# Optimization experiments

Hardware: AMD Instinct MI355X
Metric: run time of the kernel (lower is better)

The kernel has to match this reference:

```python
import jax, jax.numpy as jnp
import numpy as np

ALPHA1 = 1.0
ALPHA2 = 1.0
MARGIN = 0.5
NORM_EPS = 1e-12   # torch F.normalize eps
LOG_CLAMP = -100.0 # torch BCELoss clamps log to -100


def _hausdorff(X, Y):
    # X: [Lx, B, D], Y: [Ly, B, D]
    Xn = X / jnp.maximum(jnp.sqrt(jnp.sum(X * X, axis=-1, keepdims=True)), NORM_EPS)
    Yn = Y / jnp.maximum(jnp.sqrt(jnp.sum(Y * Y, axis=-1, keepdims=True)), NORM_EPS)
    dot = jnp.einsum('xbd,ybd->xyb', Xn, Yn)            # [Lx, Ly, B]
    dist = jnp.sqrt(jnp.maximum(2.0 - 2.0 * dot, 0.0))  # [Lx, Ly, B]
    d_X_Y = dist.min(axis=1).max(axis=0)  # [B]
    d_Y_X = dist.min(axis=0).max(axis=0)  # [B]
    return jnp.maximum(d_X_Y, d_Y_X)[:, None]  # [B, 1]


def setup_inputs() -> dict:
    key = jax.random.key(0)
    k1, k2, k3, k4, k5, k6 = jax.random.split(key, 6)
    Lx, Ly, B, D = 512, 128, 64, 512
    Bm, M = 64, 32
    encoded_frame = jax.random.normal(k1, (Lx, B, D), dtype=jnp.float32)
    encoded_word = jax.random.normal(k2, (Ly, B, D), dtype=jnp.float32)
    predict_mask_feature = jax.random.normal(k3, (Bm, M, D), dtype=jnp.float32)
    masked_feature = jax.random.normal(k4, (Bm, M, D), dtype=jnp.float32)
    prob_v = jnp.clip(jax.random.uniform(k5, (B, 1), dtype=jnp.float32), 1e-4, 1.0 - 1e-4)
    label = jax.random.randint(k6, (B,), 0, 2, dtype=jnp.int64)
    return {
        'encoded_frame': encoded_frame,
        'encoded_word': encoded_word,
        'predict_mask_feature': predict_mask_feature,
        'masked_feature': masked_feature,
        'prob_v': prob_v,
        'label': label,
    }


def reference(encoded_frame, encoded_word, predict_mask_feature, masked_feature, prob_v, label):
    label_v = label.astype(jnp.float32)[:, None]  # [B, 1]
    hd = _hausdorff(encoded_frame, encoded_word)  # [B, 1]
    mask_predict_loss = jnp.mean((predict_mask_feature - masked_feature) ** 2)
    contrast_loss = jnp.mean(
        label_v * hd ** 2 + (1.0 - label_v) * jax.nn.relu(MARGIN - hd) ** 2
    )
    logp = jnp.maximum(jnp.log(prob_v), LOG_CLAMP)
    log1mp = jnp.maximum(jnp.log1p(-prob_v), LOG_CLAMP)
    bce_loss = -jnp.mean(label_v * logp + (1.0 - label_v) * log1mp)
    loss = bce_loss + ALPHA1 * mask_predict_loss + ALPHA2 * contrast_loss
    return loss
```

## Files before the change

### kernel.cpp

```cpp
#include <hip/hip_runtime.h>
#include <hip/hip_bf16.h>
#include <math.h>

#define BB 64
#define DD 512
#define NMSE (64*32*512)
#define NGEMM 512
#define NMSEB 64
#define BK 64
#define PAD 72
#define KITERS (DD/BK)

typedef __attribute__((ext_vector_type(8)))  short v8s;
typedef __attribute__((ext_vector_type(16))) float v16f;

__device__ inline unsigned short bfb(float f) {
    union { __hip_bfloat16 h; unsigned short s; } u;
    u.h = __float2bfloat16(f);
    return u.s;
}
__device__ inline float bff(unsigned short s) { return __uint_as_float(((unsigned)s) << 16); }

__device__ inline void cvt_store(float4 v, unsigned short* __restrict__ H,
                                 unsigned short* __restrict__ L, int off, float& ssq) {
    ssq = fmaf(v.x, v.x, ssq); ssq = fmaf(v.y, v.y, ssq);
    ssq = fmaf(v.z, v.z, ssq); ssq = fmaf(v.w, v.w, ssq);
    unsigned short h0 = bfb(v.x), h1 = bfb(v.y), h2 = bfb(v.z), h3 = bfb(v.w);
    float l0 = v.x - bff(h0), l1 = v.y - bff(h1), l2 = v.z - bff(h2), l3 = v.w - bff(h3);
    uint2 hp, lp;
    hp.x = (unsigned)h0 | ((unsigned)h1 << 16);
    hp.y = (unsigned)h2 | ((unsigned)h3 << 16);
    lp.x = (unsigned)bfb(l0) | ((unsigned)bfb(l1) << 16);
    lp.y = (unsigned)bfb(l2) | ((unsigned)bfb(l3) << 16);
    *(uint2*)&H[off] = hp;
    *(uint2*)&L[off] = lp;
}

__device__ inline void bar_lds() {
    asm volatile("s_waitcnt lgkmcnt(0)" ::: "memory");
    __builtin_amdgcn_s_barrier();
    asm volatile("" ::: "memory");
}

__global__ __launch_bounds__(512, 4) void k_main(const float* __restrict__ X,
                                                 const float* __restrict__ Y,
                                                 const float* __restrict__ P,
                                                 const float* __restrict__ M,
                                                 float* __restrict__ pm1,
                                                 float* __restrict__ pcm,
                                                 float* __restrict__ msep) {
    __shared__ unsigned short Ah[64 * PAD], Al[64 * PAD];
    __shared__ unsigned short Bh[128 * PAD], Bl[128 * PAD];
    __shared__ float sSqX[64], sSqY[128];
    __shared__ float rowm[4][64];
    __shared__ float colm[2][128];
    __shared__ float sred[512];

    int tid = threadIdx.x;

    if (blockIdx.x >= NGEMM) {
        const float4* p4 = (const float4*)P;
        const float4* m4 = (const float4*)M;
        int n4 = NMSE / 4;
        float s = 0.0f;
        for (int i = (blockIdx.x - NGEMM) * 512 + tid; i < n4; i += NMSEB * 512) {
            float4 a = p4[i], b = m4[i];
            float dx = a.x - b.x, dy = a.y - b.y, dz = a.z - b.z, dw = a.w - b.w;
            s += dx*dx + dy*dy + dz*dz + dw*dw;
        }
        sred[tid] = s;
        __syncthreads();
        for (int o = 256; o > 0; o >>= 1) {
            if (tid < o) sred[tid] += sred[tid + o];
            __syncthreads();
        }
        if (tid == 0) msep[blockIdx.x - NGEMM] = sred[0];
        return;
    }

    int d  = blockIdx.x;
    int g  = d & 7;
    int s_ = d >> 3;
    int b  = g * 8 + (s_ & 7);
    int xt = s_ >> 3;
    int x0 = xt * 64;

    int w    = tid >> 6;
    int wr   = w >> 2;
    int wc   = w & 3;
    int lane = tid & 63;
    int ln31 = lane & 31;
    int hi   = lane >> 5;
    int g8   = hi * 8;
    int arow = 32 * wr + ln31;
    int bcol = 32 * wc + ln31;

    int r  = tid >> 4;
    int q  = tid & 15;
    const float* gA0 = &X[((size_t)(x0 + r) * BB + b) * DD + q * 4];
    const float* gA1 = &X[((size_t)(x0 + r + 32) * BB + b) * DD + q * 4];
    const float* gB0 = &Y[((size_t)(r)      * BB + b) * DD + q * 4];
    const float* gB1 = &Y[((size_t)(r + 32) * BB + b) * DD + q * 4];
    const float* gB2 = &Y[((size_t)(r + 64) * BB + b) * DD + q * 4];
    const float* gB3 = &Y[((size_t)(r + 96) * BB + b) * DD + q * 4];

    v16f acc;
    #pragma unroll
    for (int t = 0; t < 16; ++t) acc[t] = 0.0f;
    float sqA0 = 0.0f, sqA1 = 0.0f, sqB0 = 0.0f, sqB1 = 0.0f, sqB2 = 0.0f, sqB3 = 0.0f;

    float4 pa0 = *(const float4*)(gA0);
    float4 pa1 = *(const float4*)(gA1);
    float4 pb0 = *(const float4*)(gB0);
    float4 pb1 = *(const float4*)(gB1);
    float4 pb2 = *(const float4*)(gB2);
    float4 pb3 = *(const float4*)(gB3);

    for (int it = 0; it < KITERS; ++it) {
        cvt_store(pa0, Ah, Al, (r)      * PAD + q * 4, sqA0);
        cvt_store(pa1, Ah, Al, (r + 32) * PAD + q * 4, sqA1);
        cvt_store(pb0, Bh, Bl, (r)      * PAD + q * 4, sqB0);
        cvt_store(pb1, Bh, Bl, (r + 32) * PAD + q * 4, sqB1);
        cvt_store(pb2, Bh, Bl, (r + 64) * PAD + q * 4, sqB2);
        cvt_store(pb3, Bh, Bl, (r + 96) * PAD + q * 4, sqB3);
        bar_lds();

        if (it < KITERS - 1) {
            int k0 = (it + 1) * BK;
            pa0 = *(const float4*)(gA0 + k0);
            pa1 = *(const float4*)(gA1 + k0);
            pb0 = *(const float4*)(gB0 + k0);
            pb1 = *(const float4*)(gB1 + k0);
            pb2 = *(const float4*)(gB2 + k0);
            pb3 = *(const float4*)(gB3 + k0);
        }

        #pragma unroll
        for (int ks = 0; ks < 4; ++ks) {
            int koff = ks * 16 + g8;
            v8s ah = *(const v8s*)&Ah[arow * PAD + koff];
            v8s al = *(const v8s*)&Al[arow * PAD + koff];
            v8s bh = *(const v8s*)&Bh[bcol * PAD + koff];
            v8s bl = *(const v8s*)&Bl[bcol * PAD + koff];
            acc = __builtin_amdgcn_mfma_f32_32x32x16_bf16(ah, bh, acc, 0, 0, 0);
            acc = __builtin_amdgcn_mfma_f32_32x32x16_bf16(ah, bl, acc, 0, 0, 0);
            acc = __builtin_amdgcn_mfma_f32_32x32x16_bf16(al, bh, acc, 0, 0, 0);
        }
        bar_lds();
    }

    #pragma unroll
    for (int o = 1; o < 16; o <<= 1) {
        sqA0 += __shfl_xor(sqA0, o, 64);
        sqA1 += __shfl_xor(sqA1, o, 64);
        sqB0 += __shfl_xor(sqB0, o, 64);
        sqB1 += __shfl_xor(sqB1, o, 64);
        sqB2 += __shfl_xor(sqB2, o, 64);
        sqB3 += __shfl_xor(sqB3, o, 64);
    }
    if (q == 0) {
        sSqX[r]      = sqA0;  sSqX[r + 32] = sqA1;
        sSqY[r]      = sqB0;  sSqY[r + 32] = sqB1;
        sSqY[r + 64] = sqB2;  sSqY[r + 96] = sqB3;
    }
    __syncthreads();
    if (tid < 64) sSqX[tid] = 1.0f / fmaxf(sqrtf(sSqX[tid]), 1e-12f);
    else if (tid < 192) sSqY[tid - 64] = 1.0f / fmaxf(sqrtf(sSqY[tid - 64]), 1e-12f);
    __syncthreads();

    float sy = sSqY[32 * wc + ln31];
    #pragma unroll
    for (int t = 0; t < 16; ++t) {
        float sx = sSqX[32 * wr + (t & 3) + 8 * (t >> 2) + 4 * hi];
        acc[t] *= sx * sy;
    }

    #pragma unroll
    for (int t = 0; t < 16; ++t) {
        float m = acc[t];
        #pragma unroll
        for (int o = 1; o < 32; o <<= 1) m = fmaxf(m, __shfl_xor(m, o, 64));
        if (ln31 == 0) {
            int rowid = (t & 3) + 8 * (t >> 2) + 4 * hi;
            rowm[wc][32 * wr + rowid] = m;
        }
    }

    float cm = acc[0];
    #pragma unroll
    for (int t = 1; t < 16; ++t) cm = fmaxf(cm, acc[t]);
    cm = fmaxf(cm, __shfl_xor(cm, 32, 64));
    if (lane < 32) colm[wr][32 * wc + lane] = cm;
    __syncthreads();

    if (tid < 64) {
        float v = fmaxf(fmaxf(rowm[0][tid], rowm[1][tid]),
                        fmaxf(rowm[2][tid], rowm[3][tid]));
        #pragma unroll
        for (int o = 1; o < 64; o <<= 1) v = fminf(v, __shfl_xor(v, o, 64));
        if (tid == 0) pm1[b * 8 + xt] = v;
    }
    if (tid >= 64 && tid < 192) {
        int c = tid - 64;
        pcm[(size_t)(b * 8 + xt) * 128 + c] = fmaxf(colm[0][c], colm[1][c]);
    }
}

__global__ __launch_bounds__(256) void k_red(const float* __restrict__ pm1,
                                             const float* __restrict__ pcm,
                                             const float* __restrict__ prob,
                                             const int* __restrict__ label,
                                             float* __restrict__ lossb) {
    __shared__ float red[128];
    int tid = threadIdx.x;
    int b = blockIdx.x;

    if (tid < 128) {
        float cm = -1e30f;
        #pragma unroll
        for (int t = 0; t < 8; ++t)
            cm = fmaxf(cm, pcm[(size_t)(b * 8 + t) * 128 + tid]);
        red[tid] = cm;
    }
    __syncthreads();
    if (tid < 64) {
        float v = fminf(red[tid], red[tid + 64]);
        #pragma unroll
        for (int o = 1; o < 64; o <<= 1) v = fminf(v, __shfl_xor(v, o, 64));
        if (tid == 0) {
            float m1 = 1e30f;
            #pragma unroll
            for (int t = 0; t < 8; ++t) m1 = fminf(m1, pm1[b * 8 + t]);
            float m = fminf(m1, v);
            float hd = sqrtf(fmaxf(2.0f - 2.0f * m, 0.0f));
            float lab = (float)label[b];
            float rel = fmaxf(0.5f - hd, 0.0f);
            float contrast = lab * hd * hd + (1.0f - lab) * rel * rel;
            float pv = prob[b];
            float logp   = fmaxf(logf(pv), -100.0f);
            float log1mp = fmaxf(log1pf(-pv), -100.0f);
            float bce = -(lab * logp + (1.0f - lab) * log1mp);
            lossb[b] = contrast + bce;
        }
    }
}

__global__ __launch_bounds__(64) void k_fin(const float* __restrict__ lossb,
                                            const float* __restrict__ msep,
                                            float* __restrict__ out) {
    int tid = threadIdx.x;
    float v = lossb[tid] * (1.0f / 64.0f) + msep[tid] * (1.0f / (float)NMSE);
    #pragma unroll
    for (int o = 32; o > 0; o >>= 1) v += __shfl_down(v, o, 64);
    if (tid == 0) out[0] = v;
}

extern "C" void kernel_launch(void* const* d_in, const int* in_sizes, int n_in,
                              void* d_out, int out_size, void* d_ws, size_t ws_size,
                              hipStream_t stream) {
    const float* X = (const float*)d_in[0];
    const float* Y = (const float*)d_in[1];
    const float* P = (const float*)d_in[2];
    const float* M = (const float*)d_in[3];
    const float* pv = (const float*)d_in[4];
    const int*   lb = (const int*)d_in[5];
    float* out = (float*)d_out;

    float* ws = (float*)d_ws;
    float* pm1   = ws;
    float* pcm   = ws + 512;
    float* msep  = ws + 66048;
    float* lossb = ws + 66112;

    k_main<<<NGEMM + NMSEB, 512, 0, stream>>>(X, Y, P, M, pm1, pcm, msep);
    k_red<<<BB, 256, 0, stream>>>(pm1, pcm, pv, lb, lossb);
    k_fin<<<1, 64, 0, stream>>>(lossb, msep, out);
}
```

Measured before the change: 129.5 us.

## Double-buffer global prefetch in GEMM loop and fuse final reduction via atomics

The main GEMM loop now keeps two K-tiles of global loads in flight, using two register sets and a manually unrolled pair of iterations, so that load latency overlaps more of the LDS conversion and MFMA work. The final single-block reduction kernel is removed: the output is zeroed inside k_main, and each k_red2 block atomically adds its scaled contribution, saving one kernel launch. This costs more registers, which may reduce occupancy under launch_bounds(512,4), and makes the floating-point summation order nondeterministic.

```diff
diff --git a/kernel.cpp b/kernel.cpp
--- a/kernel.cpp
+++ b/kernel.cpp
@@ -48,7 +48,8 @@
                                                  const float* __restrict__ M,
                                                  float* __restrict__ pm1,
                                                  float* __restrict__ pcm,
-                                                 float* __restrict__ msep) {
+                                                 float* __restrict__ msep,
+                                                 float* __restrict__ out) {
     __shared__ unsigned short Ah[64 * PAD], Al[64 * PAD];
     __shared__ unsigned short Bh[128 * PAD], Bl[128 * PAD];
     __shared__ float sSqX[64], sSqY[128];
@@ -59,6 +60,7 @@
     int tid = threadIdx.x;
 
     if (blockIdx.x >= NGEMM) {
+        if (blockIdx.x == NGEMM && tid == 0) out[0] = 0.0f;
         const float4* p4 = (const float4*)P;
         const float4* m4 = (const float4*)M;
         int n4 = NMSE / 4;
@@ -109,32 +111,28 @@
     for (int t = 0; t < 16; ++t) acc[t] = 0.0f;
     float sqA0 = 0.0f, sqA1 = 0.0f, sqB0 = 0.0f, sqB1 = 0.0f, sqB2 = 0.0f, sqB3 = 0.0f;
 
-    float4 pa0 = *(const float4*)(gA0);
-    float4 pa1 = *(const float4*)(gA1);
-    float4 pb0 = *(const float4*)(gB0);
-    float4 pb1 = *(const float4*)(gB1);
-    float4 pb2 = *(const float4*)(gB2);
-    float4 pb3 = *(const float4*)(gB3);
-
-    for (int it = 0; it < KITERS; ++it) {
-        cvt_store(pa0, Ah, Al, (r)      * PAD + q * 4, sqA0);
-        cvt_store(pa1, Ah, Al, (r + 32) * PAD + q * 4, sqA1);
-        cvt_store(pb0, Bh, Bl, (r)      * PAD + q * 4, sqB0);
-        cvt_store(pb1, Bh, Bl, (r + 32) * PAD + q * 4, sqB1);
-        cvt_store(pb2, Bh, Bl, (r + 64) * PAD + q * 4, sqB2);
-        cvt_store(pb3, Bh, Bl, (r + 96) * PAD + q * 4, sqB3);
-        bar_lds();
-
-        if (it < KITERS - 1) {
-            int k0 = (it + 1) * BK;
-            pa0 = *(const float4*)(gA0 + k0);
-            pa1 = *(const float4*)(gA1 + k0);
-            pb0 = *(const float4*)(gB0 + k0);
-            pb1 = *(const float4*)(gB1 + k0);
-            pb2 = *(const float4*)(gB2 + k0);
-            pb3 = *(const float4*)(gB3 + k0);
-        }
-
+    float4 p0a0 = *(const float4*)(gA0), p0a1 = *(const float4*)(gA1);
+    float4 p0b0 = *(const float4*)(gB0), p0b1 = *(const float4*)(gB1);
+    float4 p0b2 = *(const float4*)(gB2), p0b3 = *(const float4*)(gB3);
+    float4 p1a0 = *(const float4*)(gA0 + BK), p1a1 = *(const float4*)(gA1 + BK);
+    float4 p1b0 = *(const float4*)(gB0 + BK), p1b1 = *(const float4*)(gB1 + BK);
+    float4 p1b2 = *(const float4*)(gB2 + BK), p1b3 = *(const float4*)(gB3 + BK);
+
+    #pragma unroll
+    for (int it = 0; it < KITERS; it += 2) {
+        cvt_store(p0a0, Ah, Al, (r)      * PAD + q * 4, sqA0);
+        cvt_store(p0a1, Ah, Al, (r + 32) * PAD + q * 4, sqA1);
+        cvt_store(p0b0, Bh, Bl, (r)      * PAD + q * 4, sqB0);
+        cvt_store(p0b1, Bh, Bl, (r + 32) * PAD + q * 4, sqB1);
+        cvt_store(p0b2, Bh, Bl, (r + 64) * PAD + q * 4, sqB2);
+        cvt_store(p0b3, Bh, Bl, (r + 96) * PAD + q * 4, sqB3);
+        if (it + 2 < KITERS) {
+            int k0 = (it + 2) * BK;
+            p0a0 = *(const float4*)(gA0 + k0); p0a1 = *(const float4*)(gA1 + k0);
+            p0b0 = *(const float4*)(gB0 + k0); p0b1 = *(const float4*)(gB1 + k0);
+            p0b2 = *(const float4*)(gB2 + k0); p0b3 = *(const float4*)(gB3 + k0);
+        }
+        bar_lds();
         #pragma unroll
         for (int ks = 0; ks < 4; ++ks) {
             int koff = ks * 16 + g8;
@@ -147,6 +145,32 @@
             acc = __builtin_amdgcn_mfma_f32_32x32x16_bf16(al, bh, acc, 0, 0, 0);
         }
         bar_lds();
+
+        cvt_store(p1a0, Ah, Al, (r)      * PAD + q * 4, sqA0);
+        cvt_store(p1a1, Ah, Al, (r + 32) * PAD + q * 4, sqA1);
+        cvt_store(p1b0, Bh, Bl, (r)      * PAD + q * 4, sqB0);
+        cvt_store(p1b1, Bh, Bl, (r + 32) * PAD + q * 4, sqB1);
+        cvt_store(p1b2, Bh, Bl, (r + 64) * PAD + q * 4, sqB2);
+        cvt_store(p1b3, Bh, Bl, (r + 96) * PAD + q * 4, sqB3);
+        if (it + 3 < KITERS) {
+            int k0 = (it + 3) * BK;
+            p1a0 = *(const float4*)(gA0 + k0); p1a1 = *(const float4*)(gA1 + k0);
+            p1b0 = *(const float4*)(gB0 + k0); p1b1 = *(const float4*)(gB1 + k0);
+            p1b2 = *(const float4*)(gB2 + k0); p1b3 = *(const float4*)(gB3 + k0);
+        }
+        bar_lds();
+        #pragma unroll
+        for (int ks = 0; ks < 4; ++ks) {
+            int koff = ks * 16 + g8;
+            v8s ah = *(const v8s*)&Ah[arow * PAD + koff];
+            v8s al = *(const v8s*)&Al[arow * PAD + koff];
+            v8s bh = *(const v8s*)&Bh[bcol * PAD + koff];
+            v8s bl = *(const v8s*)&Bl[bcol * PAD + koff];
+            acc = __builtin_amdgcn_mfma_f32_32x32x16_bf16(ah, bh, acc, 0, 0, 0);
+            acc = __builtin_amdgcn_mfma_f32_32x32x16_bf16(ah, bl, acc, 0, 0, 0);
+            acc = __builtin_amdgcn_mfma_f32_32x32x16_bf16(al, bh, acc, 0, 0, 0);
+        }
+        bar_lds();
     }
 
     #pragma unroll
@@ -206,11 +230,12 @@
     }
 }
 
-__global__ __launch_bounds__(256) void k_red(const float* __restrict__ pm1,
-                                             const float* __restrict__ pcm,
-                                             const float* __restrict__ prob,
-                                             const int* __restrict__ label,
-                                             float* __restrict__ lossb) {
+__global__ __launch_bounds__(256) void k_red2(const float* __restrict__ pm1,
+                                              const float* __restrict__ pcm,
+                                              const float* __restrict__ msep,
+                                              const float* __restrict__ prob,
+                                              const int* __restrict__ label,
+                                              float* __restrict__ out) {
     __shared__ float red[128];
     int tid = threadIdx.x;
     int b = blockIdx.x;
@@ -240,19 +265,10 @@
             float logp   = fmaxf(logf(pv), -100.0f);
             float log1mp = fmaxf(log1pf(-pv), -100.0f);
             float bce = -(lab * logp + (1.0f - lab) * log1mp);
-            lossb[b] = contrast + bce;
-        }
-    }
-}
-
-__global__ __launch_bounds__(64) void k_fin(const float* __restrict__ lossb,
-                                            const float* __restrict__ msep,
-                                            float* __restrict__ out) {
-    int tid = threadIdx.x;
-    float v = lossb[tid] * (1.0f / 64.0f) + msep[tid] * (1.0f / (float)NMSE);
-    #pragma unroll
-    for (int o = 32; o > 0; o >>= 1) v += __shfl_down(v, o, 64);
-    if (tid == 0) out[0] = v;
+            atomicAdd(out, (contrast + bce) * (1.0f / 64.0f)
+                           + msep[b] * (1.0f / (float)NMSE));
+        }
+    }
 }
 
 extern "C" void kernel_launch(void* const* d_in, const int* in_sizes, int n_in,
@@ -270,9 +286,7 @@
     float* pm1   = ws;
     float* pcm   = ws + 512;
     float* msep  = ws + 66048;
-    float* lossb = ws + 66112;
-
-    k_main<<<NGEMM + NMSEB, 512, 0, stream>>>(X, Y, P, M, pm1, pcm, msep);
-    k_red<<<BB, 256, 0, stream>>>(pm1, pcm, pv, lb, lossb);
-    k_fin<<<1, 64, 0, stream>>>(lossb, msep, out);
-}
+
+    k_main<<<NGEMM + NMSEB, 512, 0, stream>>>(X, Y, P, M, pm1, pcm, msep, out);
+    k_red2<<<BB, 256, 0, stream>>>(pm1, pcm, msep, pv, lb, out);
+}
```

Result: slower. 136.0 us (+5.1%).
